# Performance work log

Measured on AMD Instinct MI355X. Metric: run time of the kernel, lower is better.

Reference implementation:

```python
import jax, jax.numpy as jnp
import numpy as np

B, H, S, D = 2, 12, 2048, 64

def setup_inputs() -> dict:
    key = jax.random.key(0)
    kq, kk, kv = jax.random.split(key, 3)
    query = jax.random.normal(kq, (B, H, S, D), dtype=jnp.float32)
    k = jax.random.normal(kk, (B, H, S, D), dtype=jnp.float32)
    value = jax.random.normal(kv, (B, H, S, D), dtype=jnp.float32)
    # causal mask: 1 where allowed, 0 where masked
    mask = jnp.tril(jnp.ones((S, S), dtype=jnp.int32))[None, None, :, :]
    return {"query": query, "key": k, "value": value, "mask": mask}

def reference(query, key, value, mask):
    # qk: [B,H,S,S]
    qk = jnp.einsum('bhqd,bhkd->bhqk', query, key) / jnp.sqrt(jnp.float32(key.shape[-1]))
    # faithful quirk of the source: masked positions set to 1e-9 (not -inf)
    qk = jnp.where(mask == 0, jnp.float32(1e-9), qk)
    attention_weights = jax.nn.softmax(qk, axis=-1)
    out = jnp.einsum('bhqk,bhkd->bhqd', attention_weights, value)
    # note: self.dropout is defined but never applied in the original forward
    return out, attention_weights
```

## Files before the change

### kernel.cpp

```cpp
#include <hip/hip_runtime.h>

typedef unsigned short ushort_t;
typedef __attribute__((ext_vector_type(8))) short bf16x8;
typedef __attribute__((ext_vector_type(4))) float f32x4;

__device__ __forceinline__ unsigned short f2bf(float x) {
  union { float f; unsigned u; } v; v.f = x;
  unsigned r = v.u + 0x7fffu + ((v.u >> 16) & 1u);
  return (unsigned short)(r >> 16);
}

namespace {

constexpr int S  = 2048;
constexpr int D  = 64;
constexpr int BH = 24;
constexpr float SHIFT = 5.0f;

__global__ __launch_bounds__(256)
void cvt16(const float* __restrict__ src, ushort_t* __restrict__ dst) {
  const size_t i = (size_t)blockIdx.x * 256 + threadIdx.x;
  const float4* s4 = (const float4*)src;
  const float4 a = s4[2 * i], b = s4[2 * i + 1];
  const float x[8] = {a.x, a.y, a.z, a.w, b.x, b.y, b.z, b.w};
  bf16x8 h;
#pragma unroll
  for (int j = 0; j < 8; ++j) h[j] = (short)f2bf(x[j]);
  *(bf16x8*)(dst + 8 * i) = h;
}

__global__ __launch_bounds__(256)
void vt16(const float* __restrict__ V, ushort_t* __restrict__ vt) {
  const int bh = blockIdx.y, kc = blockIdx.x, t = threadIdx.x;
  __shared__ float tile[64][65];
  const float* vp = V + ((size_t)(bh * S + kc * 64)) * D;
#pragma unroll
  for (int i = 0; i < 4; ++i) {
    const int e4 = i * 256 + t;
    const int row = e4 >> 4, c4 = (e4 & 15) * 4;
    const float4 v = *(const float4*)(vp + row * 64 + c4);
    tile[row][c4 + 0] = v.x; tile[row][c4 + 1] = v.y;
    tile[row][c4 + 2] = v.z; tile[row][c4 + 3] = v.w;
  }
  __syncthreads();
#pragma unroll
  for (int i = 0; i < 2; ++i) {
    const int e8 = i * 256 + t;
    const int d = e8 >> 3, k8 = (e8 & 7) * 8;
    bf16x8 h;
#pragma unroll
    for (int j = 0; j < 8; ++j) h[j] = (short)f2bf(tile[k8 + j][d]);
    *(bf16x8*)(vt + ((size_t)(bh * 64 + d)) * S + kc * 64 + k8) = h;
  }
}

__global__ __launch_bounds__(64)
void csum(const float* __restrict__ V, float* __restrict__ pref) {
  const int bh = blockIdx.y, kc = blockIdx.x, d = threadIdx.x;
  const float* vp = V + ((size_t)(bh * S + kc * 64)) * D + d;
  float s = 0.f;
#pragma unroll 8
  for (int j = 0; j < 64; ++j) s += vp[(size_t)j * D];
  pref[((size_t)bh * 33 + kc) * 64 + d] = s;
}
__global__ __launch_bounds__(64)
void scan_pref(float* __restrict__ pref) {
  const int bh = blockIdx.x, d = threadIdx.x;
  float run = 0.f;
  for (int kc = 0; kc < 32; ++kc) {
    float* p = pref + ((size_t)bh * 33 + kc) * 64 + d;
    const float t = *p; *p = run; run += t;
  }
  pref[((size_t)bh * 33 + 32) * 64 + d] = run;
}

__global__ __launch_bounds__(128)
void attn3(const ushort_t* __restrict__ Qb, const ushort_t* __restrict__ Kb,
           const ushort_t* __restrict__ VTb, const float* __restrict__ pref,
           float* __restrict__ out, float* __restrict__ wts) {
  const int id  = blockIdx.x;
  const int xcd = id & 7;
  const int j   = id >> 3;
  const int bh  = xcd * 3 + (j >> 5);
  const int pp  = j & 31;

  const int tid = threadIdx.x;
  const int wv  = tid >> 6;
  const int l   = tid & 63;
  const int l15 = l & 15;
  const int g   = l >> 4;

  __shared__ __align__(16) ushort_t kbuf[2][64 * 64];
  __shared__ __align__(16) ushort_t vbuf[2][64 * 64];
  __shared__ __align__(16) ushort_t pt2[2][16][72];
  ushort_t* ptw = &pt2[wv][0][0];

  const ushort_t* Kbh = Kb  + (size_t)bh * S * D;
  const ushort_t* Vbh = VTb + (size_t)bh * D * S;
  const float cMask = __expf(1e-9f - SHIFT);

  auto stageK = [&](int buf, int kc) {
#pragma unroll
    for (int i = 0; i < 4; ++i) {
      const int gran = i * 128 + tid;
      const int row = gran >> 3, slot = gran & 7;
      const ushort_t* gp = Kbh + (size_t)(kc * 64 + row) * D + ((slot ^ (row & 7)) * 8);
      ushort_t* lp = kbuf[buf] + (size_t)(i * 128 + wv * 64) * 8;
      __builtin_amdgcn_global_load_lds((const __attribute__((address_space(1))) void*)gp,
                                       (__attribute__((address_space(3))) void*)lp, 16, 0, 0);
    }
  };
  auto stageV = [&](int buf, int kc) {
#pragma unroll
    for (int i = 0; i < 4; ++i) {
      const int gran = i * 128 + tid;
      const int row = gran >> 3, slot = gran & 7;
      const ushort_t* gp = Vbh + (size_t)row * S + kc * 64 + ((slot ^ (row & 7)) * 8);
      ushort_t* lp = vbuf[buf] + (size_t)(i * 128 + wv * 64) * 8;
      __builtin_amdgcn_global_load_lds((const __attribute__((address_space(1))) void*)gp,
                                       (__attribute__((address_space(3))) void*)lp, 16, 0, 0);
    }
  };

  for (int ti = 0; ti < 2; ++ti) {
    const int t   = ti ? (63 - pp) : pp;
    const int qw  = t * 32 + wv * 16;
    const int nch = (t >> 1) + 1;

    bf16x8 qh[2];
    {
      const size_t qo = ((size_t)(bh * S + qw + l15)) * D + g * 8;
      qh[0] = *(const bf16x8*)(Qb + qo);
      qh[1] = *(const bf16x8*)(Qb + qo + 32);
    }

    auto qk = [&](int buf, int kc, f32x4* sacc) {
#pragma unroll
      for (int kt = 0; kt < 4; ++kt) {
        sacc[kt] = f32x4{0.f, 0.f, 0.f, 0.f};
        if (kc * 64 + kt * 16 <= qw + 15) {
#pragma unroll
          for (int ks = 0; ks < 2; ++ks) {
            const int row = kt * 16 + l15;
            const bf16x8 kf = *(const bf16x8*)(kbuf[buf] + row * 64 + (((ks * 4 + g) ^ (row & 7)) * 8));
            sacc[kt] = __builtin_amdgcn_mfma_f32_16x16x32_bf16(qh[ks], kf, sacc[kt], 0, 0, 0);
          }
        }
      }
    };

    float Zp[4] = {0.f, 0.f, 0.f, 0.f};
    stageK(0, 0);
    __syncthreads();
    for (int kc = 0; kc < nch; ++kc) {
      const int cur = kc & 1;
      if (kc + 1 < nch) stageK(cur ^ 1, kc + 1);
      f32x4 sacc[4];
      qk(cur, kc, sacc);
#pragma unroll
      for (int kt = 0; kt < 4; ++kt) {
        if (kc * 64 + kt * 16 <= qw + 15) {
          const int col = kc * 64 + kt * 16 + l15;
#pragma unroll
          for (int r = 0; r < 4; ++r) {
            const float s = (col <= qw + 4 * g + r) ? sacc[kt][r] * 0.125f : 1e-9f;
            Zp[r] += __expf(s - SHIFT);
          }
        } else {
#pragma unroll
          for (int r = 0; r < 4; ++r) Zp[r] += cMask;
        }
      }
      __syncthreads();
    }

    float invZ[4], wmask[4];
#pragma unroll
    for (int r = 0; r < 4; ++r) {
#pragma unroll
      for (int off = 1; off < 16; off <<= 1) Zp[r] += __shfl_xor(Zp[r], off);
      const float Z = Zp[r] + (float)(S - nch * 64) * cMask;
      invZ[r]  = 1.f / Z;
      wmask[r] = cMask * invZ[r];
    }

    f32x4 oacc[4];
#pragma unroll
    for (int dt = 0; dt < 4; ++dt) oacc[dt] = f32x4{0.f, 0.f, 0.f, 0.f};

    stageK(0, 0); stageV(0, 0);
    __syncthreads();
    for (int kc = 0; kc < nch; ++kc) {
      const int cur = kc & 1;
      if (kc + 1 < nch) { stageK(cur ^ 1, kc + 1); stageV(cur ^ 1, kc + 1); }
      f32x4 sacc[4];
      qk(cur, kc, sacc);
#pragma unroll
      for (int kt = 0; kt < 4; ++kt) {
        const int col = kc * 64 + kt * 16 + l15;
#pragma unroll
        for (int r = 0; r < 4; ++r) {
          const int qr = qw + 4 * g + r;
          const float s = (col <= qr) ? sacc[kt][r] * 0.125f : 1e-9f;
          const float w = __expf(s - SHIFT) * invZ[r];
          __builtin_nontemporal_store(w, &wts[((size_t)(bh * S + qr)) * S + col]);
          ptw[(4 * g + r) * 72 + kt * 16 + l15] = f2bf(w);
        }
      }
      asm volatile("s_waitcnt lgkmcnt(0)" ::: "memory");
      __builtin_amdgcn_sched_barrier(0);
#pragma unroll
      for (int ks = 0; ks < 2; ++ks) {
        const bf16x8 pa = *(const bf16x8*)(ptw + l15 * 72 + ks * 32 + g * 8);
#pragma unroll
        for (int dt = 0; dt < 4; ++dt) {
          const int row = dt * 16 + l15;
          const bf16x8 vf = *(const bf16x8*)(vbuf[cur] + row * 64 + (((ks * 4 + g) ^ (row & 7)) * 8));
          oacc[dt] = __builtin_amdgcn_mfma_f32_16x16x32_bf16(pa, vf, oacc[dt], 0, 0, 0);
        }
      }
      __syncthreads();
    }

    const float* prefBH = pref + (size_t)bh * 33 * 64;
#pragma unroll
    for (int dt = 0; dt < 4; ++dt) {
      const int d = dt * 16 + l15;
      const float suf = prefBH[32 * 64 + d] - prefBH[nch * 64 + d];
#pragma unroll
      for (int r = 0; r < 4; ++r) {
        out[((size_t)(bh * S + qw + 4 * g + r)) * D + d] = oacc[dt][r] + wmask[r] * suf;
      }
    }
    const int fillStart = nch * 64;
#pragma unroll
    for (int r16 = 0; r16 < 16; ++r16) {
      const float w = __shfl(wmask[r16 & 3], (r16 >> 2) * 16);
      const f32x4 w4 = {w, w, w, w};
      float* rowp = wts + ((size_t)(bh * S + qw + r16)) * S;
      for (int c = fillStart + l * 4; c < S; c += 256) {
        __builtin_nontemporal_store(w4, (f32x4*)(rowp + c));
      }
    }
    __syncthreads();
  }
}

}

extern "C" void kernel_launch(void* const* d_in, const int* in_sizes, int n_in,
                              void* d_out, int out_size, void* d_ws, size_t ws_size,
                              hipStream_t stream) {
  const float* Q = (const float*)d_in[0];
  const float* K = (const float*)d_in[1];
  const float* V = (const float*)d_in[2];
  float* out = (float*)d_out;
  float* wts = out + (size_t)BH * S * D;

  char* ws = (char*)d_ws;
  const size_t T = (size_t)BH * S * D * 2;
  ushort_t* Qb   = (ushort_t*)(ws + 0 * T);
  ushort_t* Kb   = (ushort_t*)(ws + 1 * T);
  ushort_t* VTb  = (ushort_t*)(ws + 2 * T);
  float*    pref = (float*)(ws + 3 * T);

  cvt16<<<1536, 256, 0, stream>>>(Q, Qb);
  cvt16<<<1536, 256, 0, stream>>>(K, Kb);
  vt16<<<dim3(32, BH), 256, 0, stream>>>(V, VTb);
  csum<<<dim3(32, BH), 64, 0, stream>>>(V, pref);
  scan_pref<<<BH, 64, 0, stream>>>(pref);
  attn3<<<768, 128, 0, stream>>>(Qb, Kb, VTb, pref, out, wts);
}
```

Baseline: 134.8 us.

## Fuse preprocessing kernels and transpose QK MFMA to keep P in registers

Merges the Q and K bf16 conversion launches into one, and folds the V column-sum into the transpose kernel so there are fewer launches and V is read once. In the attention kernel the QK MFMA operands are swapped so each lane holds four consecutive keys for one query. That allows vectorized float4 nontemporal stores of the weights, packed bf16 conversion and a cross-lane shuffle to build the PV A-operand instead of going through LDS. It also permutes the tile-pair order per head group and drops a trailing barrier. The cost is extra shuffle and select instructions per chunk, and the operand swap relies on the MFMA output layout being interpreted correctly.

Measured after the change: 141.6 us. 5.1% more time.

```diff
diff --git a/kernel.cpp b/kernel.cpp
--- a/kernel.cpp
+++ b/kernel.cpp
@@ -18,11 +18,16 @@
 constexpr float SHIFT = 5.0f;
 
 __global__ __launch_bounds__(256)
-void cvt16(const float* __restrict__ src, ushort_t* __restrict__ dst) {
-  const size_t i = (size_t)blockIdx.x * 256 + threadIdx.x;
+void cvtQK(const float* __restrict__ Q, const float* __restrict__ K,
+           ushort_t* __restrict__ Qb, ushort_t* __restrict__ Kb) {
+  const int b = blockIdx.x;
+  const bool isK = (b >= 1536);
+  const float* src = isK ? K : Q;
+  ushort_t* dst = isK ? Kb : Qb;
+  const size_t i = (size_t)(isK ? b - 1536 : b) * 256 + threadIdx.x;
   const float4* s4 = (const float4*)src;
-  const float4 a = s4[2 * i], b = s4[2 * i + 1];
-  const float x[8] = {a.x, a.y, a.z, a.w, b.x, b.y, b.z, b.w};
+  const float4 a = s4[2 * i], c = s4[2 * i + 1];
+  const float x[8] = {a.x, a.y, a.z, a.w, c.x, c.y, c.z, c.w};
   bf16x8 h;
 #pragma unroll
   for (int j = 0; j < 8; ++j) h[j] = (short)f2bf(x[j]);
@@ -30,7 +35,8 @@
 }
 
 __global__ __launch_bounds__(256)
-void vt16(const float* __restrict__ V, ushort_t* __restrict__ vt) {
+void vt16c(const float* __restrict__ V, ushort_t* __restrict__ vt,
+           float* __restrict__ pref) {
   const int bh = blockIdx.y, kc = blockIdx.x, t = threadIdx.x;
   __shared__ float tile[64][65];
   const float* vp = V + ((size_t)(bh * S + kc * 64)) * D;
@@ -43,6 +49,12 @@
     tile[row][c4 + 2] = v.z; tile[row][c4 + 3] = v.w;
   }
   __syncthreads();
+  if (t < 64) {
+    float s = 0.f;
+#pragma unroll 8
+    for (int j = 0; j < 64; ++j) s += tile[j][t];
+    pref[((size_t)bh * 33 + kc) * 64 + t] = s;
+  }
 #pragma unroll
   for (int i = 0; i < 2; ++i) {
     const int e8 = i * 256 + t;
@@ -54,15 +66,6 @@
   }
 }
 
-__global__ __launch_bounds__(64)
-void csum(const float* __restrict__ V, float* __restrict__ pref) {
-  const int bh = blockIdx.y, kc = blockIdx.x, d = threadIdx.x;
-  const float* vp = V + ((size_t)(bh * S + kc * 64)) * D + d;
-  float s = 0.f;
-#pragma unroll 8
-  for (int j = 0; j < 64; ++j) s += vp[(size_t)j * D];
-  pref[((size_t)bh * 33 + kc) * 64 + d] = s;
-}
 __global__ __launch_bounds__(64)
 void scan_pref(float* __restrict__ pref) {
   const int bh = blockIdx.x, d = threadIdx.x;
@@ -75,14 +78,15 @@
 }
 
 __global__ __launch_bounds__(128)
-void attn3(const ushort_t* __restrict__ Qb, const ushort_t* __restrict__ Kb,
+void attn4(const ushort_t* __restrict__ Qb, const ushort_t* __restrict__ Kb,
            const ushort_t* __restrict__ VTb, const float* __restrict__ pref,
            float* __restrict__ out, float* __restrict__ wts) {
   const int id  = blockIdx.x;
   const int xcd = id & 7;
   const int j   = id >> 3;
-  const int bh  = xcd * 3 + (j >> 5);
-  const int pp  = j & 31;
+  const int grp = j >> 5;
+  const int bh  = xcd * 3 + grp;
+  const int pp  = ((j & 31) * 11 + grp * 7) & 31;
 
   const int tid = threadIdx.x;
   const int wv  = tid >> 6;
@@ -92,8 +96,6 @@
 
   __shared__ __align__(16) ushort_t kbuf[2][64 * 64];
   __shared__ __align__(16) ushort_t vbuf[2][64 * 64];
-  __shared__ __align__(16) ushort_t pt2[2][16][72];
-  ushort_t* ptw = &pt2[wv][0][0];
 
   const ushort_t* Kbh = Kb  + (size_t)bh * S * D;
   const ushort_t* Vbh = VTb + (size_t)bh * D * S;
@@ -126,10 +128,11 @@
     const int t   = ti ? (63 - pp) : pp;
     const int qw  = t * 32 + wv * 16;
     const int nch = (t >> 1) + 1;
+    const int q   = qw + l15;
 
     bf16x8 qh[2];
     {
-      const size_t qo = ((size_t)(bh * S + qw + l15)) * D + g * 8;
+      const size_t qo = ((size_t)(bh * S + q)) * D + g * 8;
       qh[0] = *(const bf16x8*)(Qb + qo);
       qh[1] = *(const bf16x8*)(Qb + qo + 32);
     }
@@ -143,13 +146,13 @@
           for (int ks = 0; ks < 2; ++ks) {
             const int row = kt * 16 + l15;
             const bf16x8 kf = *(const bf16x8*)(kbuf[buf] + row * 64 + (((ks * 4 + g) ^ (row & 7)) * 8));
-            sacc[kt] = __builtin_amdgcn_mfma_f32_16x16x32_bf16(qh[ks], kf, sacc[kt], 0, 0, 0);
+            sacc[kt] = __builtin_amdgcn_mfma_f32_16x16x32_bf16(kf, qh[ks], sacc[kt], 0, 0, 0);
           }
         }
       }
     };
 
-    float Zp[4] = {0.f, 0.f, 0.f, 0.f};
+    float Zp = 0.f;
     stageK(0, 0);
     __syncthreads();
     for (int kc = 0; kc < nch; ++kc) {
@@ -160,29 +163,23 @@
 #pragma unroll
       for (int kt = 0; kt < 4; ++kt) {
         if (kc * 64 + kt * 16 <= qw + 15) {
-          const int col = kc * 64 + kt * 16 + l15;
+          const int kbase = kc * 64 + kt * 16 + 4 * g;
 #pragma unroll
           for (int r = 0; r < 4; ++r) {
-            const float s = (col <= qw + 4 * g + r) ? sacc[kt][r] * 0.125f : 1e-9f;
-            Zp[r] += __expf(s - SHIFT);
+            const float s = (kbase + r <= q) ? sacc[kt][r] * 0.125f : 1e-9f;
+            Zp += __expf(s - SHIFT);
           }
         } else {
-#pragma unroll
-          for (int r = 0; r < 4; ++r) Zp[r] += cMask;
+          Zp += 4.f * cMask;
         }
       }
       __syncthreads();
     }
-
-    float invZ[4], wmask[4];
-#pragma unroll
-    for (int r = 0; r < 4; ++r) {
-#pragma unroll
-      for (int off = 1; off < 16; off <<= 1) Zp[r] += __shfl_xor(Zp[r], off);
-      const float Z = Zp[r] + (float)(S - nch * 64) * cMask;
-      invZ[r]  = 1.f / Z;
-      wmask[r] = cMask * invZ[r];
-    }
+    Zp += __shfl_xor(Zp, 16);
+    Zp += __shfl_xor(Zp, 32);
+    const float Z     = Zp + (float)(S - nch * 64) * cMask;
+    const float invZ  = 1.f / Z;
+    const float wmask = cMask * invZ;
 
     f32x4 oacc[4];
 #pragma unroll
@@ -195,23 +192,45 @@
       if (kc + 1 < nch) { stageK(cur ^ 1, kc + 1); stageV(cur ^ 1, kc + 1); }
       f32x4 sacc[4];
       qk(cur, kc, sacc);
+
+      int pk[4][2];
 #pragma unroll
       for (int kt = 0; kt < 4; ++kt) {
-        const int col = kc * 64 + kt * 16 + l15;
-#pragma unroll
-        for (int r = 0; r < 4; ++r) {
-          const int qr = qw + 4 * g + r;
-          const float s = (col <= qr) ? sacc[kt][r] * 0.125f : 1e-9f;
-          const float w = __expf(s - SHIFT) * invZ[r];
-          __builtin_nontemporal_store(w, &wts[((size_t)(bh * S + qr)) * S + col]);
-          ptw[(4 * g + r) * 72 + kt * 16 + l15] = f2bf(w);
-        }
-      }
-      asm volatile("s_waitcnt lgkmcnt(0)" ::: "memory");
-      __builtin_amdgcn_sched_barrier(0);
+        const int kbase = kc * 64 + kt * 16 + 4 * g;
+        f32x4 w4;
+        if (kc * 64 + kt * 16 <= qw + 15) {
+#pragma unroll
+          for (int r = 0; r < 4; ++r) {
+            const float s = (kbase + r <= q) ? sacc[kt][r] * 0.125f : 1e-9f;
+            w4[r] = __expf(s - SHIFT) * invZ;
+          }
+        } else {
+          w4 = f32x4{wmask, wmask, wmask, wmask};
+        }
+        __builtin_nontemporal_store(w4, (f32x4*)&wts[((size_t)(bh * S + q)) * S + kbase]);
+        asm("v_cvt_pk_bf16_f32 %0, %1, %2" : "=v"(pk[kt][0]) : "v"(w4[0]), "v"(w4[1]));
+        asm("v_cvt_pk_bf16_f32 %0, %1, %2" : "=v"(pk[kt][1]) : "v"(w4[2]), "v"(w4[3]));
+      }
+
+      const int srcA = l15 + ((g & 1) * 2) * 16;
+      const int srcB = srcA + 16;
+      const bool hi = (g & 2) != 0;
 #pragma unroll
       for (int ks = 0; ks < 2; ++ks) {
-        const bf16x8 pa = *(const bf16x8*)(ptw + l15 * 72 + ks * 32 + g * 8);
+        const int a0 = __shfl(pk[ks * 2][0], srcA);
+        const int a1 = __shfl(pk[ks * 2][1], srcA);
+        const int a2 = __shfl(pk[ks * 2][0], srcB);
+        const int a3 = __shfl(pk[ks * 2][1], srcB);
+        const int b0 = __shfl(pk[ks * 2 + 1][0], srcA);
+        const int b1 = __shfl(pk[ks * 2 + 1][1], srcA);
+        const int b2 = __shfl(pk[ks * 2 + 1][0], srcB);
+        const int b3 = __shfl(pk[ks * 2 + 1][1], srcB);
+        union { int d[4]; bf16x8 v; } u;
+        u.d[0] = hi ? b0 : a0;
+        u.d[1] = hi ? b1 : a1;
+        u.d[2] = hi ? b2 : a2;
+        u.d[3] = hi ? b3 : a3;
+        const bf16x8 pa = u.v;
 #pragma unroll
         for (int dt = 0; dt < 4; ++dt) {
           const int row = dt * 16 + l15;
@@ -222,6 +241,9 @@
       __syncthreads();
     }
 
+    float wm[4];
+#pragma unroll
+    for (int r = 0; r < 4; ++r) wm[r] = __shfl(wmask, 4 * g + r);
     const float* prefBH = pref + (size_t)bh * 33 * 64;
 #pragma unroll
     for (int dt = 0; dt < 4; ++dt) {
@@ -229,20 +251,19 @@
       const float suf = prefBH[32 * 64 + d] - prefBH[nch * 64 + d];
 #pragma unroll
       for (int r = 0; r < 4; ++r) {
-        out[((size_t)(bh * S + qw + 4 * g + r)) * D + d] = oacc[dt][r] + wmask[r] * suf;
+        out[((size_t)(bh * S + qw + 4 * g + r)) * D + d] = oacc[dt][r] + wm[r] * suf;
       }
     }
     const int fillStart = nch * 64;
 #pragma unroll
     for (int r16 = 0; r16 < 16; ++r16) {
-      const float w = __shfl(wmask[r16 & 3], (r16 >> 2) * 16);
+      const float w = __shfl(wmask, r16);
       const f32x4 w4 = {w, w, w, w};
       float* rowp = wts + ((size_t)(bh * S + qw + r16)) * S;
       for (int c = fillStart + l * 4; c < S; c += 256) {
         __builtin_nontemporal_store(w4, (f32x4*)(rowp + c));
       }
     }
-    __syncthreads();
   }
 }
 
@@ -264,10 +285,8 @@
   ushort_t* VTb  = (ushort_t*)(ws + 2 * T);
   float*    pref = (float*)(ws + 3 * T);
 
-  cvt16<<<1536, 256, 0, stream>>>(Q, Qb);
-  cvt16<<<1536, 256, 0, stream>>>(K, Kb);
-  vt16<<<dim3(32, BH), 256, 0, stream>>>(V, VTb);
-  csum<<<dim3(32, BH), 64, 0, stream>>>(V, pref);
+  cvtQK<<<3072, 256, 0, stream>>>(Q, K, Qb, Kb);
+  vt16c<<<dim3(32, BH), 256, 0, stream>>>(V, VTb, pref);
   scan_pref<<<BH, 64, 0, stream>>>(pref);
-  attn3<<<768, 128, 0, stream>>>(Qb, Kb, VTb, pref, out, wts);
-}
+  attn4<<<768, 128, 0, stream>>>(Qb, Kb, VTb, pref, out, wts);
+}
```
